# Performance work log

Hardware: AMD Instinct MI355X
Metric: run time of the kernel (lower is better)

The kernel has to match this reference:

```python
import jax, jax.numpy as jnp
import numpy as np

B, L, C, H = 1, 256, 128, 4  # batch, seq len, c_z, n_heads
D = C // H                    # head_dim = 32


def setup_inputs() -> dict:
    key = jax.random.key(0)
    ks = jax.random.split(key, 8)
    w = lambda k, shape: jax.random.normal(k, shape, jnp.float32) * 0.02
    return {
        "pair": jax.random.normal(ks[0], (B, L, L, C), jnp.float32),
        "ln_g": jnp.ones((C,), jnp.float32),
        "ln_b": jnp.zeros((C,), jnp.float32),
        "Wq": w(ks[1], (C, C)),
        "Wk": w(ks[2], (C, C)),
        "Wv": w(ks[3], (C, C)),
        "Wbias": w(ks[4], (C, H)),
        "Wo": w(ks[5], (C, C)),
        "bo": jnp.zeros((C,), jnp.float32),
        "Wg": w(ks[6], (C, C)),
        "bg": jnp.zeros((C,), jnp.float32),
    }


def reference(pair, ln_g, ln_b, Wq, Wk, Wv, Wbias, Wo, bo, Wg, bg):
    # mode == 'starting': no transpose of pair
    # LayerNorm over c_z
    mu = jnp.mean(pair, axis=-1, keepdims=True)
    var = jnp.mean(jnp.square(pair - mu), axis=-1, keepdims=True)
    z = (pair - mu) * jax.lax.rsqrt(var + 1e-5) * ln_g + ln_b

    q = (z @ Wq).reshape(B, L, L, H, D)
    k = (z @ Wk).reshape(B, L, L, H, D)
    v = (z @ Wv).reshape(B, L, L, H, D)

    # logits: [B, H, i, j, k], scaled by 1/sqrt(head_dim)
    attn = jnp.einsum('bijhd,bikhd->bhijk', q, k) * (1.0 / np.sqrt(D).astype(np.float32))
    # pairwise additive bias: bias_proj(z) -> [B, L, L, H] -> [B, H, 1, j, k]
    bias = jnp.einsum('bjkc,ch->bhjk', z, Wbias)[:, :, None, :, :]
    attn = jax.nn.softmax(attn + bias, axis=-1)

    out = jnp.einsum('bhijk,bikhd->bijhd', attn, v).reshape(B, L, L, C)
    result = pair + jax.nn.sigmoid(pair @ Wg + bg) * (out @ Wo + bo)
    return result
```

## Files before the change

kernel.cpp:

```cpp
#include <hip/hip_runtime.h>
#include <cstdint>
#include <cstddef>

#define L_ 256
#define C_ 128
#define H_ 4
#define D_ 32
#define NP_ (L_ * L_)

typedef unsigned short u16;
typedef uint32_t u32;
typedef __attribute__((ext_vector_type(8))) short bf16x8;
typedef __attribute__((ext_vector_type(4))) float f32x4;

__device__ __forceinline__ float bflo(u32 u) { union { u32 i; float f; } v; v.i = u << 16; return v.f; }
__device__ __forceinline__ float bfhi(u32 u) { union { u32 i; float f; } v; v.i = u & 0xffff0000u; return v.f; }
__device__ __forceinline__ u16 f2b(float f) {
    u32 x = __float_as_uint(f);
    return (u16)((x + 0x7fffu + ((x >> 16) & 1u)) >> 16);
}
__device__ __forceinline__ u32 pk2(float lo, float hi) {
    return ((u32)f2b(hi) << 16) | (u32)f2b(lo);
}
__device__ __forceinline__ bf16x8 pack8(float4 a, float4 b) {
    union { u32 u[4]; bf16x8 v; } r;
    r.u[0] = pk2(a.x, a.y); r.u[1] = pk2(a.z, a.w);
    r.u[2] = pk2(b.x, b.y); r.u[3] = pk2(b.z, b.w);
    return r.v;
}

__global__ __launch_bounds__(256) void k_prep(
    const float* __restrict__ Wq, const float* __restrict__ Wk, const float* __restrict__ Wv,
    const float* __restrict__ Wo, const float* __restrict__ Wg,
    const float* __restrict__ Wbias, u16* __restrict__ Wt, float* __restrict__ WbT)
{
    __shared__ float tile[64][65];
    const int b = blockIdx.x, t = threadIdx.x;
    if (b < 20) {
        const int mat = b >> 2, tl = b & 3, tr = tl >> 1, tc = tl & 1;
        const float* W = (mat == 0) ? Wq : (mat == 1) ? Wk : (mat == 2) ? Wv : (mat == 3) ? Wo : Wg;
        const float s = (mat == 0) ? 0.2550680544705824f : 1.f;
        const int rlo = t >> 6, col = t & 63;
        #pragma unroll
        for (int m = 0; m < 16; ++m) {
            int row = m * 4 + rlo;
            tile[row][col] = W[(size_t)(tr * 64 + row) * C_ + tc * 64 + col];
        }
        __syncthreads();
        #pragma unroll
        for (int m = 0; m < 16; ++m) {
            int n = tc * 64 + m * 4 + rlo;
            int c = tr * 64 + col;
            Wt[mat * 16384 + n * C_ + c] = f2b(tile[col][m * 4 + rlo] * s);
        }
    } else {
        #pragma unroll
        for (int m = 0; m < 2; ++m) {
            int idx = m * 256 + t;
            int h = idx >> 7, c = idx & 127;
            WbT[h * C_ + c] = Wbias[c * H_ + h] * 1.4426950408889634f;
        }
    }
}

__global__ __launch_bounds__(256) void k_lnmm(
    const float* __restrict__ pair, const float* __restrict__ ln_g, const float* __restrict__ ln_b,
    const u16* __restrict__ Wt, const float* __restrict__ WbT,
    u16* __restrict__ qh, u16* __restrict__ kh, u16* __restrict__ vh,
    float* __restrict__ biasN)
{
    __shared__ u16 zsh[64][136];

    const int t  = threadIdx.x;
    const int p0 = blockIdx.x * 64;
    const int row = t >> 2, seg = t & 3;

    float4 xv[8];
    float sum = 0.f, ss = 0.f;
    #pragma unroll
    for (int i = 0; i < 8; ++i) {
        int c = (seg + 4 * i) * 4;
        float4 x = *(const float4*)(pair + (size_t)(p0 + row) * C_ + c);
        xv[i] = x;
        sum += x.x + x.y + x.z + x.w;
        ss  += x.x * x.x + x.y * x.y + x.z * x.z + x.w * x.w;
    }
    sum += __shfl_xor(sum, 1); sum += __shfl_xor(sum, 2);
    ss  += __shfl_xor(ss, 1);  ss  += __shfl_xor(ss, 2);
    float mu  = sum * (1.0f / C_);
    float var = ss * (1.0f / C_) - mu * mu;
    float rs  = rsqrtf(fmaxf(var, 0.f) + 1e-5f);

    #pragma unroll
    for (int i = 0; i < 8; ++i) {
        int c = (seg + 4 * i) * 4;
        float4 g4 = *(const float4*)(ln_g + c);
        float4 b4 = *(const float4*)(ln_b + c);
        float4 x  = xv[i];
        float z0 = (x.x - mu) * rs * g4.x + b4.x;
        float z1 = (x.y - mu) * rs * g4.y + b4.y;
        float z2 = (x.z - mu) * rs * g4.z + b4.z;
        float z3 = (x.w - mu) * rs * g4.w + b4.w;
        *(u32*)&zsh[row][c]     = pk2(z0, z1);
        *(u32*)&zsh[row][c + 2] = pk2(z2, z3);
    }
    __syncthreads();

    const int w    = t >> 6;
    const int l15  = t & 15;
    const int quad = (t >> 4) & 3;

    bf16x8 zf[4][4];
    #pragma unroll
    for (int jt = 0; jt < 4; ++jt)
        #pragma unroll
        for (int kc = 0; kc < 4; ++kc)
            zf[jt][kc] = *(const bf16x8*)&zsh[jt * 16 + l15][kc * 32 + quad * 8];

    #pragma unroll
    for (int k = 0; k < 6; ++k) {
        const int tt = w * 6 + k;
        const int mat = tt >> 3, mt = tt & 7;
        f32x4 acc0 = {0.f,0.f,0.f,0.f}, acc1 = acc0, acc2 = acc0, acc3 = acc0;
        #pragma unroll
        for (int kc = 0; kc < 4; ++kc) {
            bf16x8 af = *(const bf16x8*)(Wt + (size_t)tt * 2048 + (size_t)l15 * 128 + kc * 32 + quad * 8);
            acc0 = __builtin_amdgcn_mfma_f32_16x16x32_bf16(af, zf[0][kc], acc0, 0, 0, 0);
            acc1 = __builtin_amdgcn_mfma_f32_16x16x32_bf16(af, zf[1][kc], acc1, 0, 0, 0);
            acc2 = __builtin_amdgcn_mfma_f32_16x16x32_bf16(af, zf[2][kc], acc2, 0, 0, 0);
            acc3 = __builtin_amdgcn_mfma_f32_16x16x32_bf16(af, zf[3][kc], acc3, 0, 0, 0);
        }
        u16* dst = (mat == 0) ? qh : (mat == 1) ? kh : vh;
        const int hh = mt >> 1;
        const int cb = (mt & 1) * 16 + quad * 4;
        f32x4 accs[4] = {acc0, acc1, acc2, acc3};
        #pragma unroll
        for (int jt = 0; jt < 4; ++jt) {
            const int p = p0 + jt * 16 + l15;
            *(uint2*)(dst + ((size_t)hh * NP_ + p) * D_ + cb) =
                make_uint2(pk2(accs[jt][0], accs[jt][1]), pk2(accs[jt][2], accs[jt][3]));
        }
    }

    {
        float a = 0.f;
        #pragma unroll
        for (int c8 = 0; c8 < C_; c8 += 8) {
            uint4 zz = *(const uint4*)&zsh[row][c8];
            float4 wb0 = *(const float4*)(WbT + seg * C_ + c8);
            float4 wb1 = *(const float4*)(WbT + seg * C_ + c8 + 4);
            a += bflo(zz.x) * wb0.x + bfhi(zz.x) * wb0.y
               + bflo(zz.y) * wb0.z + bfhi(zz.y) * wb0.w
               + bflo(zz.z) * wb1.x + bfhi(zz.z) * wb1.y
               + bflo(zz.w) * wb1.z + bfhi(zz.w) * wb1.w;
        }
        const int p = p0 + row;
        biasN[(size_t)seg * NP_ + p] = a;
    }
}

__global__ __launch_bounds__(256, 4) void k_attn(
    u16* __restrict__ qh, const u16* __restrict__ kh, const u16* __restrict__ vh,
    const float* __restrict__ biasN)
{
    __shared__ u16 Vsh[D_ * 264];
    __shared__ u16 Psh[4][16][40];

    const int t = threadIdx.x;
    const int i = blockIdx.x >> 2;
    const int h = blockIdx.x & 3;
    const int w    = t >> 6;
    const int l15  = t & 15;
    const int quad = (t >> 4) & 3;
    const int jbase = w * 64;

    const u16* Kg = kh + ((size_t)h * NP_ + i * L_) * D_;
    const u16* Vg = vh + ((size_t)h * NP_ + i * L_) * D_;
    u16*       Qg = qh + ((size_t)h * NP_ + i * L_) * D_;

    #pragma unroll
    for (int jj = 0; jj < 4; ++jj) {
        int idx = t + jj * 256;
        int r = idx >> 2, sg = idx & 3;
        union { uint4 q; u16 s[8]; } u;
        u.q = *(const uint4*)(Vg + r * D_ + sg * 8);
        #pragma unroll
        for (int m = 0; m < 8; ++m) Vsh[(sg * 8 + m) * 264 + r] = u.s[m];
    }

    bf16x8 qf[4];
    #pragma unroll
    for (int jt = 0; jt < 4; ++jt)
        qf[jt] = *(const bf16x8*)(Qg + (size_t)(jbase + jt * 16 + l15) * D_ + quad * 8);

    __syncthreads();

    const f32x4 z4 = {0.f, 0.f, 0.f, 0.f};
    f32x4 oacc[4][2], osum[4];
    #pragma unroll
    for (int jt = 0; jt < 4; ++jt) {
        oacc[jt][0] = z4; oacc[jt][1] = z4; osum[jt] = z4;
    }

    bf16x8 onesb;
    { union { u32 u[4]; bf16x8 v; } ob;
      ob.u[0] = ob.u[1] = ob.u[2] = ob.u[3] = 0x3F803F80u; onesb = ob.v; }

    const float* bN = biasN + (size_t)h * NP_;

    bf16x8 kb0 = *(const bf16x8*)(Kg + (size_t)l15 * D_ + quad * 8);
    bf16x8 kb1 = *(const bf16x8*)(Kg + (size_t)(16 + l15) * D_ + quad * 8);

    for (int kc = 0; kc < 8; ++kc) {
        bf16x8 nb0, nb1;
        if (kc < 7) {
            nb0 = *(const bf16x8*)(Kg + (size_t)((kc + 1) * 32 + l15) * D_ + quad * 8);
            nb1 = *(const bf16x8*)(Kg + (size_t)((kc + 1) * 32 + 16 + l15) * D_ + quad * 8);
        }
        bf16x8 vb0 = *(const bf16x8*)&Vsh[l15 * 264 + kc * 32 + quad * 8];
        bf16x8 vb1 = *(const bf16x8*)&Vsh[(16 + l15) * 264 + kc * 32 + quad * 8];

        #pragma unroll
        for (int jt = 0; jt < 4; ++jt) {
            f32x4 s0 = __builtin_amdgcn_mfma_f32_16x16x32_bf16(kb0, qf[jt], z4, 0, 0, 0);
            f32x4 s1 = __builtin_amdgcn_mfma_f32_16x16x32_bf16(kb1, qf[jt], z4, 0, 0, 0);

            const float* bp = bN + (size_t)(jbase + jt * 16 + l15) * L_ + kc * 32 + quad * 4;
            float4 bv0 = *(const float4*)bp;
            float4 bv1 = *(const float4*)(bp + 16);

            float e0[4], e1[4];
            e0[0] = __builtin_amdgcn_exp2f(s0[0] + bv0.x);
            e0[1] = __builtin_amdgcn_exp2f(s0[1] + bv0.y);
            e0[2] = __builtin_amdgcn_exp2f(s0[2] + bv0.z);
            e0[3] = __builtin_amdgcn_exp2f(s0[3] + bv0.w);
            e1[0] = __builtin_amdgcn_exp2f(s1[0] + bv1.x);
            e1[1] = __builtin_amdgcn_exp2f(s1[1] + bv1.y);
            e1[2] = __builtin_amdgcn_exp2f(s1[2] + bv1.z);
            e1[3] = __builtin_amdgcn_exp2f(s1[3] + bv1.w);

            u32 w0, w1, w2, w3;
            asm("v_cvt_pk_bf16_f32 %0, %1, %2" : "=v"(w0) : "v"(e0[0]), "v"(e0[1]));
            asm("v_cvt_pk_bf16_f32 %0, %1, %2" : "=v"(w1) : "v"(e0[2]), "v"(e0[3]));
            asm("v_cvt_pk_bf16_f32 %0, %1, %2" : "=v"(w2) : "v"(e1[0]), "v"(e1[1]));
            asm("v_cvt_pk_bf16_f32 %0, %1, %2" : "=v"(w3) : "v"(e1[2]), "v"(e1[3]));
            *(uint2*)&Psh[w][l15][quad * 4]      = make_uint2(w0, w1);
            *(uint2*)&Psh[w][l15][16 + quad * 4] = make_uint2(w2, w3);

            bf16x8 pa = *(const bf16x8*)&Psh[w][l15][quad * 8];
            oacc[jt][0] = __builtin_amdgcn_mfma_f32_16x16x32_bf16(pa, vb0,   oacc[jt][0], 0, 0, 0);
            oacc[jt][1] = __builtin_amdgcn_mfma_f32_16x16x32_bf16(pa, vb1,   oacc[jt][1], 0, 0, 0);
            osum[jt]    = __builtin_amdgcn_mfma_f32_16x16x32_bf16(pa, onesb, osum[jt],    0, 0, 0);
        }
        kb0 = nb0; kb1 = nb1;
    }

    #pragma unroll
    for (int jt = 0; jt < 4; ++jt) {
        #pragma unroll
        for (int r = 0; r < 4; ++r) {
            float rn = 1.f / osum[jt][r];
            size_t rowo = (size_t)(jbase + jt * 16 + quad * 4 + r) * D_;
            Qg[rowo + l15]      = f2b(oacc[jt][0][r] * rn);
            Qg[rowo + 16 + l15] = f2b(oacc[jt][1][r] * rn);
        }
    }
}

__global__ __launch_bounds__(256) void k_out(
    const u16* __restrict__ aoh, const float* __restrict__ pair,
    const u16* __restrict__ Wt, const float* __restrict__ bo,
    const float* __restrict__ bg, float* __restrict__ out)
{
    const int t  = threadIdx.x;
    const int p0 = blockIdx.x * 128;
    const int w    = t >> 6;
    const int l15  = t & 15;
    const int quad = (t >> 4) & 3;

    bf16x8 aof[2][4], pf[2][4];
    int prow[2];
    #pragma unroll
    for (int g = 0; g < 2; ++g) {
        prow[g] = p0 + w * 32 + g * 16 + l15;
        #pragma unroll
        for (int kc = 0; kc < 4; ++kc) {
            aof[g][kc] = *(const bf16x8*)(aoh + ((size_t)kc * NP_ + prow[g]) * D_ + quad * 8);
            const float* pp = pair + (size_t)prow[g] * C_ + kc * 32 + quad * 8;
            pf[g][kc] = pack8(*(const float4*)pp, *(const float4*)(pp + 4));
        }
    }

    const u16* WoT = Wt + 3 * 16384;
    const u16* WgT = Wt + 4 * 16384;

    #pragma unroll
    for (int nt = 0; nt < 8; ++nt) {
        f32x4 accO0 = {0.f,0.f,0.f,0.f}, accO1 = accO0, accG0 = accO0, accG1 = accO0;
        #pragma unroll
        for (int kc = 0; kc < 4; ++kc) {
            bf16x8 awo = *(const bf16x8*)(WoT + (size_t)(nt * 16 + l15) * 128 + kc * 32 + quad * 8);
            bf16x8 awg = *(const bf16x8*)(WgT + (size_t)(nt * 16 + l15) * 128 + kc * 32 + quad * 8);
            accO0 = __builtin_amdgcn_mfma_f32_16x16x32_bf16(awo, aof[0][kc], accO0, 0, 0, 0);
            accO1 = __builtin_amdgcn_mfma_f32_16x16x32_bf16(awo, aof[1][kc], accO1, 0, 0, 0);
            accG0 = __builtin_amdgcn_mfma_f32_16x16x32_bf16(awg, pf[0][kc],  accG0, 0, 0, 0);
            accG1 = __builtin_amdgcn_mfma_f32_16x16x32_bf16(awg, pf[1][kc],  accG1, 0, 0, 0);
        }
        const int ch = nt * 16 + quad * 4;
        float4 bo4 = *(const float4*)(bo + ch);
        float4 bg4 = *(const float4*)(bg + ch);
        f32x4 aO[2] = {accO0, accO1}, aG[2] = {accG0, accG1};
        #pragma unroll
        for (int g = 0; g < 2; ++g) {
            float4 pr = *(const float4*)(pair + (size_t)prow[g] * C_ + ch);
            float4 r;
            r.x = pr.x + (1.f / (1.f + __expf(-(aG[g][0] + bg4.x)))) * (aO[g][0] + bo4.x);
            r.y = pr.y + (1.f / (1.f + __expf(-(aG[g][1] + bg4.y)))) * (aO[g][1] + bo4.y);
            r.z = pr.z + (1.f / (1.f + __expf(-(aG[g][2] + bg4.z)))) * (aO[g][2] + bo4.z);
            r.w = pr.w + (1.f / (1.f + __expf(-(aG[g][3] + bg4.w)))) * (aO[g][3] + bo4.w);
            *(float4*)(out + (size_t)prow[g] * C_ + ch) = r;
        }
    }
}

extern "C" void kernel_launch(void* const* d_in, const int* in_sizes, int n_in,
                              void* d_out, int out_size, void* d_ws, size_t ws_size,
                              hipStream_t stream) {
    const float* pair  = (const float*)d_in[0];
    const float* ln_g  = (const float*)d_in[1];
    const float* ln_b  = (const float*)d_in[2];
    const float* Wq    = (const float*)d_in[3];
    const float* Wk    = (const float*)d_in[4];
    const float* Wv    = (const float*)d_in[5];
    const float* Wbias = (const float*)d_in[6];
    const float* Wo    = (const float*)d_in[7];
    const float* bo    = (const float*)d_in[8];
    const float* Wg    = (const float*)d_in[9];
    const float* bg    = (const float*)d_in[10];
    float* out = (float*)d_out;

    float* biasN = (float*)d_ws;
    u16* qh = (u16*)(biasN + (size_t)H_ * NP_);
    u16* kh = qh + (size_t)NP_ * C_;
    u16* vh = kh + (size_t)NP_ * C_;
    u16* Wt = vh + (size_t)NP_ * C_;
    float* WbT = (float*)(Wt + 5 * 16384);

    k_prep<<<21, 256, 0, stream>>>(Wq, Wk, Wv, Wo, Wg, Wbias, Wt, WbT);
    k_lnmm<<<NP_ / 64, 256, 0, stream>>>(pair, ln_g, ln_b, Wt, WbT, qh, kh, vh, biasN);
    k_attn<<<L_ * H_, 256, 0, stream>>>(qh, kh, vh, biasN);
    k_out<<<NP_ / 128, 256, 0, stream>>>(qh, pair, Wt, bo, bg, out);
}
```

Measured before the change: 204.0 us.

## Fuse attention and output projection into one kernel with per-row blocks

Merges the attention kernel and the output-projection/gating kernel into a single 1024-thread kernel. Each block handles one row i for all four heads and stages the attention output in shared memory, so it never round-trips through global memory. The output GEMM then reads that tile from LDS. Costs include higher LDS use (about 150KB per block), only 256 blocks on the device, and a block-wide barrier between the two phases, all of which can cut occupancy.

```diff
diff --git a/kernel.cpp b/kernel.cpp
--- a/kernel.cpp
+++ b/kernel.cpp
@@ -159,33 +159,40 @@
     }
 }
 
-__global__ __launch_bounds__(256, 4) void k_attn(
-    u16* __restrict__ qh, const u16* __restrict__ kh, const u16* __restrict__ vh,
-    const float* __restrict__ biasN)
+__global__ __launch_bounds__(1024)
+__attribute__((amdgpu_waves_per_eu(4, 4)))
+void k_ao(
+    const u16* __restrict__ qh, const u16* __restrict__ kh, const u16* __restrict__ vh,
+    const float* __restrict__ biasN, const float* __restrict__ pair,
+    const u16* __restrict__ Wt, const float* __restrict__ bo,
+    const float* __restrict__ bg, float* __restrict__ out)
 {
-    __shared__ u16 Vsh[D_ * 264];
-    __shared__ u16 Psh[4][16][40];
+    __shared__ u16 Vsh[4 * 32 * 264];
+    __shared__ u16 Psh[16][16][40];
+    __shared__ u16 ao_sh[256 * 136];
 
     const int t = threadIdx.x;
-    const int i = blockIdx.x >> 2;
-    const int h = blockIdx.x & 3;
-    const int w    = t >> 6;
+    const int i = blockIdx.x;
+    const int wave = t >> 6;
+    const int h    = wave >> 2;
+    const int ww   = wave & 3;
     const int l15  = t & 15;
     const int quad = (t >> 4) & 3;
-    const int jbase = w * 64;
+    const int jbase = ww * 64;
 
     const u16* Kg = kh + ((size_t)h * NP_ + i * L_) * D_;
-    const u16* Vg = vh + ((size_t)h * NP_ + i * L_) * D_;
-    u16*       Qg = qh + ((size_t)h * NP_ + i * L_) * D_;
+    const u16* Qg = qh + ((size_t)h * NP_ + i * L_) * D_;
 
     #pragma unroll
     for (int jj = 0; jj < 4; ++jj) {
-        int idx = t + jj * 256;
-        int r = idx >> 2, sg = idx & 3;
+        int idx = t + jj * 1024;
+        int hs = idx >> 10, rem = idx & 1023;
+        int r = rem >> 2, sg = rem & 3;
+        const u16* Vg = vh + ((size_t)hs * NP_ + i * L_) * D_;
         union { uint4 q; u16 s[8]; } u;
         u.q = *(const uint4*)(Vg + r * D_ + sg * 8);
         #pragma unroll
-        for (int m = 0; m < 8; ++m) Vsh[(sg * 8 + m) * 264 + r] = u.s[m];
+        for (int m = 0; m < 8; ++m) Vsh[hs * 8448 + (sg * 8 + m) * 264 + r] = u.s[m];
     }
 
     bf16x8 qf[4];
@@ -207,6 +214,7 @@
       ob.u[0] = ob.u[1] = ob.u[2] = ob.u[3] = 0x3F803F80u; onesb = ob.v; }
 
     const float* bN = biasN + (size_t)h * NP_;
+    const u16* Vs = Vsh + h * 8448;
 
     bf16x8 kb0 = *(const bf16x8*)(Kg + (size_t)l15 * D_ + quad * 8);
     bf16x8 kb1 = *(const bf16x8*)(Kg + (size_t)(16 + l15) * D_ + quad * 8);
@@ -217,8 +225,8 @@
             nb0 = *(const bf16x8*)(Kg + (size_t)((kc + 1) * 32 + l15) * D_ + quad * 8);
             nb1 = *(const bf16x8*)(Kg + (size_t)((kc + 1) * 32 + 16 + l15) * D_ + quad * 8);
         }
-        bf16x8 vb0 = *(const bf16x8*)&Vsh[l15 * 264 + kc * 32 + quad * 8];
-        bf16x8 vb1 = *(const bf16x8*)&Vsh[(16 + l15) * 264 + kc * 32 + quad * 8];
+        bf16x8 vb0 = *(const bf16x8*)&Vs[l15 * 264 + kc * 32 + quad * 8];
+        bf16x8 vb1 = *(const bf16x8*)&Vs[(16 + l15) * 264 + kc * 32 + quad * 8];
 
         #pragma unroll
         for (int jt = 0; jt < 4; ++jt) {
@@ -244,10 +252,10 @@
             asm("v_cvt_pk_bf16_f32 %0, %1, %2" : "=v"(w1) : "v"(e0[2]), "v"(e0[3]));
             asm("v_cvt_pk_bf16_f32 %0, %1, %2" : "=v"(w2) : "v"(e1[0]), "v"(e1[1]));
             asm("v_cvt_pk_bf16_f32 %0, %1, %2" : "=v"(w3) : "v"(e1[2]), "v"(e1[3]));
-            *(uint2*)&Psh[w][l15][quad * 4]      = make_uint2(w0, w1);
-            *(uint2*)&Psh[w][l15][16 + quad * 4] = make_uint2(w2, w3);
-
-            bf16x8 pa = *(const bf16x8*)&Psh[w][l15][quad * 8];
+            *(uint2*)&Psh[wave][l15][quad * 4]      = make_uint2(w0, w1);
+            *(uint2*)&Psh[wave][l15][16 + quad * 4] = make_uint2(w2, w3);
+
+            bf16x8 pa = *(const bf16x8*)&Psh[wave][l15][quad * 8];
             oacc[jt][0] = __builtin_amdgcn_mfma_f32_16x16x32_bf16(pa, vb0,   oacc[jt][0], 0, 0, 0);
             oacc[jt][1] = __builtin_amdgcn_mfma_f32_16x16x32_bf16(pa, vb1,   oacc[jt][1], 0, 0, 0);
             osum[jt]    = __builtin_amdgcn_mfma_f32_16x16x32_bf16(pa, onesb, osum[jt],    0, 0, 0);
@@ -260,35 +268,23 @@
         #pragma unroll
         for (int r = 0; r < 4; ++r) {
             float rn = 1.f / osum[jt][r];
-            size_t rowo = (size_t)(jbase + jt * 16 + quad * 4 + r) * D_;
-            Qg[rowo + l15]      = f2b(oacc[jt][0][r] * rn);
-            Qg[rowo + 16 + l15] = f2b(oacc[jt][1][r] * rn);
-        }
-    }
-}
-
-__global__ __launch_bounds__(256) void k_out(
-    const u16* __restrict__ aoh, const float* __restrict__ pair,
-    const u16* __restrict__ Wt, const float* __restrict__ bo,
-    const float* __restrict__ bg, float* __restrict__ out)
-{
-    const int t  = threadIdx.x;
-    const int p0 = blockIdx.x * 128;
-    const int w    = t >> 6;
-    const int l15  = t & 15;
-    const int quad = (t >> 4) & 3;
-
-    bf16x8 aof[2][4], pf[2][4];
-    int prow[2];
-    #pragma unroll
-    for (int g = 0; g < 2; ++g) {
-        prow[g] = p0 + w * 32 + g * 16 + l15;
-        #pragma unroll
-        for (int kc = 0; kc < 4; ++kc) {
-            aof[g][kc] = *(const bf16x8*)(aoh + ((size_t)kc * NP_ + prow[g]) * D_ + quad * 8);
-            const float* pp = pair + (size_t)prow[g] * C_ + kc * 32 + quad * 8;
-            pf[g][kc] = pack8(*(const float4*)pp, *(const float4*)(pp + 4));
-        }
+            int prow = jbase + jt * 16 + quad * 4 + r;
+            ao_sh[prow * 136 + h * 32 + l15]      = f2b(oacc[jt][0][r] * rn);
+            ao_sh[prow * 136 + h * 32 + 16 + l15] = f2b(oacc[jt][1][r] * rn);
+        }
+    }
+
+    __syncthreads();
+
+    const int prow_l = wave * 16 + l15;
+    const int pg     = i * L_ + prow_l;
+
+    bf16x8 aof[4], pf[4];
+    #pragma unroll
+    for (int kc = 0; kc < 4; ++kc) {
+        aof[kc] = *(const bf16x8*)&ao_sh[prow_l * 136 + kc * 32 + quad * 8];
+        const float* pp = pair + (size_t)pg * C_ + kc * 32 + quad * 8;
+        pf[kc] = pack8(*(const float4*)pp, *(const float4*)(pp + 4));
     }
 
     const u16* WoT = Wt + 3 * 16384;
@@ -296,30 +292,24 @@
 
     #pragma unroll
     for (int nt = 0; nt < 8; ++nt) {
-        f32x4 accO0 = {0.f,0.f,0.f,0.f}, accO1 = accO0, accG0 = accO0, accG1 = accO0;
+        f32x4 accO = {0.f,0.f,0.f,0.f}, accG = accO;
         #pragma unroll
         for (int kc = 0; kc < 4; ++kc) {
             bf16x8 awo = *(const bf16x8*)(WoT + (size_t)(nt * 16 + l15) * 128 + kc * 32 + quad * 8);
             bf16x8 awg = *(const bf16x8*)(WgT + (size_t)(nt * 16 + l15) * 128 + kc * 32 + quad * 8);
-            accO0 = __builtin_amdgcn_mfma_f32_16x16x32_bf16(awo, aof[0][kc], accO0, 0, 0, 0);
-            accO1 = __builtin_amdgcn_mfma_f32_16x16x32_bf16(awo, aof[1][kc], accO1, 0, 0, 0);
-            accG0 = __builtin_amdgcn_mfma_f32_16x16x32_bf16(awg, pf[0][kc],  accG0, 0, 0, 0);
-            accG1 = __builtin_amdgcn_mfma_f32_16x16x32_bf16(awg, pf[1][kc],  accG1, 0, 0, 0);
+            accO = __builtin_amdgcn_mfma_f32_16x16x32_bf16(awo, aof[kc], accO, 0, 0, 0);
+            accG = __builtin_amdgcn_mfma_f32_16x16x32_bf16(awg, pf[kc],  accG, 0, 0, 0);
         }
         const int ch = nt * 16 + quad * 4;
         float4 bo4 = *(const float4*)(bo + ch);
         float4 bg4 = *(const float4*)(bg + ch);
-        f32x4 aO[2] = {accO0, accO1}, aG[2] = {accG0, accG1};
-        #pragma unroll
-        for (int g = 0; g < 2; ++g) {
-            float4 pr = *(const float4*)(pair + (size_t)prow[g] * C_ + ch);
-            float4 r;
-            r.x = pr.x + (1.f / (1.f + __expf(-(aG[g][0] + bg4.x)))) * (aO[g][0] + bo4.x);
-            r.y = pr.y + (1.f / (1.f + __expf(-(aG[g][1] + bg4.y)))) * (aO[g][1] + bo4.y);
-            r.z = pr.z + (1.f / (1.f + __expf(-(aG[g][2] + bg4.z)))) * (aO[g][2] + bo4.z);
-            r.w = pr.w + (1.f / (1.f + __expf(-(aG[g][3] + bg4.w)))) * (aO[g][3] + bo4.w);
-            *(float4*)(out + (size_t)prow[g] * C_ + ch) = r;
-        }
+        float4 pr  = *(const float4*)(pair + (size_t)pg * C_ + ch);
+        float4 r;
+        r.x = pr.x + (1.f / (1.f + __expf(-(accG[0] + bg4.x)))) * (accO[0] + bo4.x);
+        r.y = pr.y + (1.f / (1.f + __expf(-(accG[1] + bg4.y)))) * (accO[1] + bo4.y);
+        r.z = pr.z + (1.f / (1.f + __expf(-(accG[2] + bg4.z)))) * (accO[2] + bo4.z);
+        r.w = pr.w + (1.f / (1.f + __expf(-(accG[3] + bg4.w)))) * (accO[3] + bo4.w);
+        *(float4*)(out + (size_t)pg * C_ + ch) = r;
     }
 }
 
@@ -348,6 +338,5 @@
 
     k_prep<<<21, 256, 0, stream>>>(Wq, Wk, Wv, Wo, Wg, Wbias, Wt, WbT);
     k_lnmm<<<NP_ / 64, 256, 0, stream>>>(pair, ln_g, ln_b, Wt, WbT, qh, kh, vh, biasN);
-    k_attn<<<L_ * H_, 256, 0, stream>>>(qh, kh, vh, biasN);
-    k_out<<<NP_ / 128, 256, 0, stream>>>(qh, pair, Wt, bo, bg, out);
-}
+    k_ao<<<L_, 1024, 0, stream>>>(qh, kh, vh, biasN, pair, Wt, bo, bg, out);
+}
```

After: 204.5 us. Within noise of the previous version (+0.3%).
